# Kernel optimization log

Measured on AMD Instinct MI355X. Metric: run time of the kernel, lower is better.

Reference implementation:

```python
import jax, jax.numpy as jnp
import numpy as np

N_NODES = 100000
N_EDGES = 1600000
ATOM_DIM = 16
POS_DIM = 3
HID = 128


def _linear_init(key, fan_in, fan_out):
    # torch nn.Linear default: U(-1/sqrt(fan_in), 1/sqrt(fan_in)) for W and b
    kw, kb = jax.random.split(key)
    bound = 1.0 / np.sqrt(fan_in)
    W = jax.random.uniform(kw, (fan_in, fan_out), jnp.float32, -bound, bound)
    b = jax.random.uniform(kb, (fan_out,), jnp.float32, -bound, bound)
    return W, b


def setup_inputs() -> dict:
    key = jax.random.key(0)
    ks = jax.random.split(key, 8)
    x = jax.random.normal(ks[0], (N_NODES, ATOM_DIM), jnp.float32)
    pos = jax.random.normal(ks[1], (N_NODES, POS_DIM), jnp.float32)
    edge_index = jax.random.randint(ks[2], (2, N_EDGES), 0, N_NODES, jnp.int64 if jax.config.jax_enable_x64 else jnp.int32)
    Wa, ba = _linear_init(ks[3], ATOM_DIM, HID)
    Wp, bp = _linear_init(ks[4], POS_DIM, HID)
    W1, b1 = _linear_init(ks[5], 2 * HID + 1, HID)
    W2, b2 = _linear_init(ks[6], HID, HID)
    W3, b3 = _linear_init(ks[7], HID, 4)
    return {"x": x, "pos": pos, "edge_index": edge_index,
            "Wa": Wa, "ba": ba, "Wp": Wp, "bp": bp,
            "W1": W1, "b1": b1, "W2": W2, "b2": b2, "W3": W3, "b3": b3}


def reference(x, pos, edge_index, Wa, ba, Wp, bp, W1, b1, W2, b2, W3, b3):
    # node embeddings: atom_emb + pos_emb, [N, HID]
    node_emb = (x @ Wa + ba) + (pos @ Wp + bp)
    src, dst = edge_index[0], edge_index[1]
    source_emb = node_emb[src]            # [E, HID]
    target_emb = node_emb[dst]            # [E, HID]
    diff = pos[src] - pos[dst]            # [E, 3]
    distances = jnp.linalg.norm(diff, axis=-1, keepdims=True)  # [E, 1]
    edge_input = jnp.concatenate([source_emb, target_emb, distances], axis=-1)  # [E, 2*HID+1]
    h = jax.nn.silu(edge_input @ W1 + b1)
    h = jax.nn.silu(h @ W2 + b2)
    bond_logits = h @ W3 + b3             # [E, 4]
    return bond_logits
```

## Files before the change

kernel.cpp:

```cpp
#include <hip/hip_runtime.h>
#include <hip/hip_bf16.h>
#include <hip/hip_fp16.h>

typedef _Float16 half8 __attribute__((ext_vector_type(8)));
typedef _Float16 half4 __attribute__((ext_vector_type(4)));
typedef __fp16 fp16x2 __attribute__((ext_vector_type(2)));
typedef float floatx4 __attribute__((ext_vector_type(4)));

#define HID 128
#define TILE_M 64

__device__ __forceinline__ float fast_silu(float v) {
    float e = __expf(-v);
    return v * __builtin_amdgcn_rcpf(1.f + e);
}

__device__ __forceinline__ unsigned int pk2(float a, float b) {
    fp16x2 h = __builtin_amdgcn_cvt_pkrtz(a, b);
    return __builtin_bit_cast(unsigned int, h);
}

__device__ __forceinline__ void barrier_lds_only() {
    asm volatile("s_waitcnt lgkmcnt(0)\n\ts_barrier" ::: "memory");
}

#define LDO 136
__global__ __launch_bounds__(256) void node_emb_kernel(
    const float* __restrict__ x, const float* __restrict__ pos,
    const float* __restrict__ Wa, const float* __restrict__ ba,
    const float* __restrict__ Wp, const float* __restrict__ bp,
    _Float16* __restrict__ nodeEmb, int N)
{
    __shared__ __align__(16) _Float16 sOut[64 * LDO];
    const int t    = threadIdx.x;
    const int wave = t >> 6;
    const int lane = t & 63;
    const int quad = lane >> 4;
    const int l16  = lane & 15;

    half8 wf[2];
    floatx4 bias[2];
    #pragma unroll
    for (int ct = 0; ct < 2; ++ct) {
        int col = wave * 32 + ct * 16 + l16;
        #pragma unroll
        for (int j = 0; j < 8; ++j) {
            int k = quad * 8 + j;
            float w = 0.f;
            if (k < 16) w = Wa[k * HID + col];
            else if (k < 19) w = Wp[(k - 16) * HID + col];
            wf[ct][j] = (_Float16)w;
        }
        #pragma unroll
        for (int i = 0; i < 4; ++i) {
            int c2 = wave * 32 + ct * 16 + quad * 4 + i;
            bias[ct][i] = ba[c2] + bp[c2];
        }
    }

    int nTiles = (N + 63) >> 6;
    for (int tile = blockIdx.x; tile < nTiles; tile += gridDim.x) {
        int base = tile * 64;
        half8 af[4];
        #pragma unroll
        for (int rt = 0; rt < 4; ++rt) {
            int node = base + rt * 16 + l16;
            int nd = node < N ? node : N - 1;
            half8 a = (half8){0, 0, 0, 0, 0, 0, 0, 0};
            if (quad < 2) {
                const float* xp = x + (size_t)nd * 16 + quad * 8;
                float4 v0 = *(const float4*)xp;
                float4 v1 = *(const float4*)(xp + 4);
                a[0] = (_Float16)v0.x; a[1] = (_Float16)v0.y;
                a[2] = (_Float16)v0.z; a[3] = (_Float16)v0.w;
                a[4] = (_Float16)v1.x; a[5] = (_Float16)v1.y;
                a[6] = (_Float16)v1.z; a[7] = (_Float16)v1.w;
            } else if (quad == 2) {
                const float* pp = pos + (size_t)nd * 3;
                a[0] = (_Float16)pp[0]; a[1] = (_Float16)pp[1]; a[2] = (_Float16)pp[2];
            }
            af[rt] = a;
        }
        #pragma unroll
        for (int ct = 0; ct < 2; ++ct)
            #pragma unroll
            for (int rt = 0; rt < 4; ++rt) {
                floatx4 d = bias[ct];
                d = __builtin_amdgcn_mfma_f32_16x16x32_f16(wf[ct], af[rt], d, 0, 0, 0);
                half4 hv;
                hv[0] = (_Float16)d[0]; hv[1] = (_Float16)d[1];
                hv[2] = (_Float16)d[2]; hv[3] = (_Float16)d[3];
                *(half4*)&sOut[(rt * 16 + l16) * LDO + wave * 32 + ct * 16 + quad * 4] = hv;
            }
        __syncthreads();
        #pragma unroll
        for (int p = 0; p < 4; ++p) {
            int idx = p * 256 + t;
            int r = idx >> 4, c = idx & 15;
            int node = base + r;
            if (node < N)
                *(half8*)(nodeEmb + (size_t)node * HID + c * 8) =
                    *(const half8*)&sOut[r * LDO + c * 8];
        }
        __syncthreads();
    }
}

__global__ __launch_bounds__(256, 2) void edge_mlp_kernel(
    const _Float16* __restrict__ nodeEmb,
    const float* __restrict__ pos,
    const int* __restrict__ eidx,
    const float* __restrict__ W1, const float* __restrict__ b1,
    const float* __restrict__ W2, const float* __restrict__ b2,
    const float* __restrict__ W3, const float* __restrict__ b3,
    float* __restrict__ out, int E, int nTiles)
{
    __shared__ __align__(16) _Float16 sA[2 * TILE_M * HID];
    __shared__ __align__(16) _Float16 sH1[TILE_M * HID];
    __shared__ __align__(16) _Float16 sH2[TILE_M * HID];
    __shared__ float sDist[TILE_M];

    const int t    = threadIdx.x;
    const int wave = t >> 6;
    const int lane = t & 63;
    const int quad = lane >> 4;
    const int l16  = lane & 15;
    const int colbase = wave * 32;

    half8 w1f[8][2];
    half8 w2f[4][2];
    half8 w3f[4];
    float w1c[2][4], b1f[2][4], b2f[2][4];
    #pragma unroll
    for (int ct = 0; ct < 2; ++ct) {
        int col = colbase + ct * 16 + l16;
        #pragma unroll
        for (int kc = 0; kc < 8; ++kc)
            #pragma unroll
            for (int j = 0; j < 8; ++j)
                w1f[kc][ct][j] = (_Float16)W1[(kc * 32 + quad * 8 + j) * HID + col];
        #pragma unroll
        for (int kc = 0; kc < 4; ++kc)
            #pragma unroll
            for (int j = 0; j < 8; ++j)
                w2f[kc][ct][j] = (_Float16)W2[(kc * 32 + quad * 8 + j) * HID + col];
        #pragma unroll
        for (int i = 0; i < 4; ++i) {
            int c2 = colbase + ct * 16 + quad * 4 + i;
            w1c[ct][i] = W1[256 * HID + c2];
            b1f[ct][i] = b1[c2];
            b2f[ct][i] = b2[c2];
        }
    }
    #pragma unroll
    for (int kc = 0; kc < 4; ++kc)
        #pragma unroll
        for (int j = 0; j < 8; ++j)
            w3f[kc][j] = (_Float16)W3[(kc * 32 + quad * 8 + j) * 4 + (l16 & 3)];
    const float b3v0 = b3[0], b3v1 = b3[1], b3v2 = b3[2], b3v3 = b3[3];

    int nid[8];
    float dpre = 0.f;

    auto load_nid = [&](int tl) {
        int eb = tl * TILE_M;
        #pragma unroll
        for (int i = 0; i < 8; ++i) {
            int cid = i * 256 + t;
            int row = cid >> 4;
            int r   = row & 63;
            int e   = eb + r; if (e >= E) e = E - 1;
            nid[i] = (row >> 6) ? eidx[(size_t)E + e] : eidx[e];
        }
    };
    auto load_dist = [&](int tl) -> float {
        if (t >= TILE_M) return 0.f;
        int e = tl * TILE_M + t; if (e >= E) e = E - 1;
        int s = eidx[e], d = eidx[(size_t)E + e];
        float dx = pos[3 * (size_t)s]     - pos[3 * (size_t)d];
        float dy = pos[3 * (size_t)s + 1] - pos[3 * (size_t)d + 1];
        float dz = pos[3 * (size_t)s + 2] - pos[3 * (size_t)d + 2];
        return sqrtf(dx * dx + dy * dy + dz * dz);
    };
    auto dma_issue = [&]() {
        #pragma unroll
        for (int i = 0; i < 8; ++i) {
            int cid = i * 256 + t;
            int row = cid >> 4;
            int cg  = (cid & 15) ^ (row & 15);
            const _Float16* gp = nodeEmb + (size_t)nid[i] * HID + cg * 8;
            __builtin_amdgcn_global_load_lds(
                (__attribute__((address_space(1))) void*)gp,
                (__attribute__((address_space(3))) void*)&sA[(i * 256 + (t & 192)) * 8],
                16, 0, 0);
        }
    };

    bool havePrev = false;
    int prevEbase = 0;
    int tile = blockIdx.x;
    if (tile < nTiles) {
        load_nid(tile);
        dpre = load_dist(tile);
        dma_issue();
    }

    for (; tile < nTiles; tile += gridDim.x) {
        const int ebase = tile * TILE_M;
        if (t < TILE_M) sDist[t] = dpre;
        __syncthreads();

        if (havePrev) {
            floatx4 acc3 = (floatx4){0.f, 0.f, 0.f, 0.f};
            #pragma unroll
            for (int kc = 0; kc < 4; ++kc) {
                int slot = ((kc * 4 + quad) ^ l16) * 8;
                half8 h = *(const half8*)&sH2[(wave * 16 + l16) * HID + slot];
                acc3 = __builtin_amdgcn_mfma_f32_16x16x32_f16(w3f[kc], h, acc3, 0, 0, 0);
            }
            if (quad == 0) {
                int e = prevEbase + wave * 16 + l16;
                if (e < E) {
                    float4 o = {acc3[0] + b3v0, acc3[1] + b3v1,
                                acc3[2] + b3v2, acc3[3] + b3v3};
                    *(float4*)&out[(size_t)e * 4] = o;
                }
            }
        }

        int nxt = tile + gridDim.x;
        if (nxt < nTiles) {
            load_nid(nxt);
            dpre = load_dist(nxt);
        }

        floatx4 acc[2][4];
        #pragma unroll
        for (int ct = 0; ct < 2; ++ct)
            #pragma unroll
            for (int rt = 0; rt < 4; ++rt) {
                acc[ct][rt][0] = b1f[ct][0]; acc[ct][rt][1] = b1f[ct][1];
                acc[ct][rt][2] = b1f[ct][2]; acc[ct][rt][3] = b1f[ct][3];
            }
        #pragma unroll
        for (int kc = 0; kc < 8; ++kc) {
            int hf   = kc >> 2;
            int cg   = (kc & 3) * 4 + quad;
            int slot = (cg ^ l16) * 8;
            const _Float16* base = &sA[(hf * TILE_M + l16) * HID + slot];
            half8 a0 = *(const half8*)(base + 0 * 16 * HID);
            half8 a1 = *(const half8*)(base + 1 * 16 * HID);
            half8 a2 = *(const half8*)(base + 2 * 16 * HID);
            half8 a3 = *(const half8*)(base + 3 * 16 * HID);
            acc[0][0] = __builtin_amdgcn_mfma_f32_16x16x32_f16(w1f[kc][0], a0, acc[0][0], 0, 0, 0);
            acc[0][1] = __builtin_amdgcn_mfma_f32_16x16x32_f16(w1f[kc][0], a1, acc[0][1], 0, 0, 0);
            acc[0][2] = __builtin_amdgcn_mfma_f32_16x16x32_f16(w1f[kc][0], a2, acc[0][2], 0, 0, 0);
            acc[0][3] = __builtin_amdgcn_mfma_f32_16x16x32_f16(w1f[kc][0], a3, acc[0][3], 0, 0, 0);
            acc[1][0] = __builtin_amdgcn_mfma_f32_16x16x32_f16(w1f[kc][1], a0, acc[1][0], 0, 0, 0);
            acc[1][1] = __builtin_amdgcn_mfma_f32_16x16x32_f16(w1f[kc][1], a1, acc[1][1], 0, 0, 0);
            acc[1][2] = __builtin_amdgcn_mfma_f32_16x16x32_f16(w1f[kc][1], a2, acc[1][2], 0, 0, 0);
            acc[1][3] = __builtin_amdgcn_mfma_f32_16x16x32_f16(w1f[kc][1], a3, acc[1][3], 0, 0, 0);
        }
        #pragma unroll
        for (int rt = 0; rt < 4; ++rt) {
            int m = rt * 16 + l16;
            float d = sDist[m];
            #pragma unroll
            for (int ct = 0; ct < 2; ++ct) {
                float v0 = fast_silu(fmaf(d, w1c[ct][0], acc[ct][rt][0]));
                float v1 = fast_silu(fmaf(d, w1c[ct][1], acc[ct][rt][1]));
                float v2 = fast_silu(fmaf(d, w1c[ct][2], acc[ct][rt][2]));
                float v3 = fast_silu(fmaf(d, w1c[ct][3], acc[ct][rt][3]));
                uint2 w;
                w.x = pk2(v0, v1);
                w.y = pk2(v2, v3);
                int cgb  = wave * 4 + ct * 2 + (quad >> 1);
                int slot = cgb ^ l16;
                *(uint2*)&sH1[m * HID + slot * 8 + (quad & 1) * 4] = w;
            }
        }
        barrier_lds_only();

        if (nxt < nTiles) dma_issue();

        floatx4 acc2[2][4];
        #pragma unroll
        for (int ct = 0; ct < 2; ++ct)
            #pragma unroll
            for (int rt = 0; rt < 4; ++rt) {
                acc2[ct][rt][0] = b2f[ct][0]; acc2[ct][rt][1] = b2f[ct][1];
                acc2[ct][rt][2] = b2f[ct][2]; acc2[ct][rt][3] = b2f[ct][3];
            }
        #pragma unroll
        for (int kc = 0; kc < 4; ++kc) {
            int slot = ((kc * 4 + quad) ^ l16) * 8;
            half8 a0 = *(const half8*)&sH1[(0 * 16 + l16) * HID + slot];
            half8 a1 = *(const half8*)&sH1[(1 * 16 + l16) * HID + slot];
            half8 a2 = *(const half8*)&sH1[(2 * 16 + l16) * HID + slot];
            half8 a3 = *(const half8*)&sH1[(3 * 16 + l16) * HID + slot];
            acc2[0][0] = __builtin_amdgcn_mfma_f32_16x16x32_f16(w2f[kc][0], a0, acc2[0][0], 0, 0, 0);
            acc2[0][1] = __builtin_amdgcn_mfma_f32_16x16x32_f16(w2f[kc][0], a1, acc2[0][1], 0, 0, 0);
            acc2[0][2] = __builtin_amdgcn_mfma_f32_16x16x32_f16(w2f[kc][0], a2, acc2[0][2], 0, 0, 0);
            acc2[0][3] = __builtin_amdgcn_mfma_f32_16x16x32_f16(w2f[kc][0], a3, acc2[0][3], 0, 0, 0);
            acc2[1][0] = __builtin_amdgcn_mfma_f32_16x16x32_f16(w2f[kc][1], a0, acc2[1][0], 0, 0, 0);
            acc2[1][1] = __builtin_amdgcn_mfma_f32_16x16x32_f16(w2f[kc][1], a1, acc2[1][1], 0, 0, 0);
            acc2[1][2] = __builtin_amdgcn_mfma_f32_16x16x32_f16(w2f[kc][1], a2, acc2[1][2], 0, 0, 0);
            acc2[1][3] = __builtin_amdgcn_mfma_f32_16x16x32_f16(w2f[kc][1], a3, acc2[1][3], 0, 0, 0);
        }
        #pragma unroll
        for (int rt = 0; rt < 4; ++rt) {
            int m = rt * 16 + l16;
            #pragma unroll
            for (int ct = 0; ct < 2; ++ct) {
                float v0 = fast_silu(acc2[ct][rt][0]);
                float v1 = fast_silu(acc2[ct][rt][1]);
                float v2 = fast_silu(acc2[ct][rt][2]);
                float v3 = fast_silu(acc2[ct][rt][3]);
                uint2 w;
                w.x = pk2(v0, v1);
                w.y = pk2(v2, v3);
                int cgb  = wave * 4 + ct * 2 + (quad >> 1);
                int slot = cgb ^ l16;
                *(uint2*)&sH2[m * HID + slot * 8 + (quad & 1) * 4] = w;
            }
        }
        havePrev = true;
        prevEbase = ebase;
    }

    if (havePrev) {
        __syncthreads();
        floatx4 acc3 = (floatx4){0.f, 0.f, 0.f, 0.f};
        #pragma unroll
        for (int kc = 0; kc < 4; ++kc) {
            int slot = ((kc * 4 + quad) ^ l16) * 8;
            half8 h = *(const half8*)&sH2[(wave * 16 + l16) * HID + slot];
            acc3 = __builtin_amdgcn_mfma_f32_16x16x32_f16(w3f[kc], h, acc3, 0, 0, 0);
        }
        if (quad == 0) {
            int e = prevEbase + wave * 16 + l16;
            if (e < E) {
                float4 o = {acc3[0] + b3v0, acc3[1] + b3v1,
                            acc3[2] + b3v2, acc3[3] + b3v3};
                *(float4*)&out[(size_t)e * 4] = o;
            }
        }
    }
}

extern "C" void kernel_launch(void* const* d_in, const int* in_sizes, int n_in,
                              void* d_out, int out_size, void* d_ws, size_t ws_size,
                              hipStream_t stream) {
    const float* x   = (const float*)d_in[0];
    const float* pos = (const float*)d_in[1];
    const int*  eidx = (const int*)d_in[2];
    const float* Wa = (const float*)d_in[3];
    const float* ba = (const float*)d_in[4];
    const float* Wp = (const float*)d_in[5];
    const float* bp = (const float*)d_in[6];
    const float* W1 = (const float*)d_in[7];
    const float* b1 = (const float*)d_in[8];
    const float* W2 = (const float*)d_in[9];
    const float* b2 = (const float*)d_in[10];
    const float* W3 = (const float*)d_in[11];
    const float* b3 = (const float*)d_in[12];
    float* out = (float*)d_out;

    int N = in_sizes[0] / 16;
    int E = in_sizes[2] / 2;

    _Float16* nodeEmb = (_Float16*)d_ws;

    int nodeTiles = (N + 63) / 64;
    node_emb_kernel<<<nodeTiles, 256, 0, stream>>>(x, pos, Wa, ba, Wp, bp, nodeEmb, N);

    int nTiles = (E + TILE_M - 1) / TILE_M;
    edge_mlp_kernel<<<512, 256, 0, stream>>>(nodeEmb, pos, eidx,
                                             W1, b1, W2, b2, W3, b3,
                                             out, E, nTiles);
}
```

Baseline: 342.8 us.

## Double-buffer edge input tile and alias hidden activations into consumed buffer

The separate H1/H2 shared buffers are removed and the LDS is split into two ping-pong tile buffers of the same total size. The layer-1 and layer-2 activations now overwrite the current tile's gathered node embeddings once layer 1 has read them. This lets the gather of the next tile's embeddings start right after the layer-1 MFMAs, so it overlaps with SiLU, layer 2 and the layer-3 epilogue. It adds an extra barrier per tile and relies on careful aliasing: the previous tile's H2 must be fully read before the new gather overwrites that buffer.

```diff
diff --git a/kernel.cpp b/kernel.cpp
--- a/kernel.cpp
+++ b/kernel.cpp
@@ -9,6 +9,8 @@
 
 #define HID 128
 #define TILE_M 64
+#define TSZ (2 * TILE_M * HID)
+#define H2OFF (TILE_M * HID)
 
 __device__ __forceinline__ float fast_silu(float v) {
     float e = __expf(-v);
@@ -115,9 +117,7 @@
     const float* __restrict__ W3, const float* __restrict__ b3,
     float* __restrict__ out, int E, int nTiles)
 {
-    __shared__ __align__(16) _Float16 sA[2 * TILE_M * HID];
-    __shared__ __align__(16) _Float16 sH1[TILE_M * HID];
-    __shared__ __align__(16) _Float16 sH2[TILE_M * HID];
+    __shared__ __align__(16) _Float16 sA[2 * TSZ];
     __shared__ float sDist[TILE_M];
 
     const int t    = threadIdx.x;
@@ -182,7 +182,7 @@
         float dz = pos[3 * (size_t)s + 2] - pos[3 * (size_t)d + 2];
         return sqrtf(dx * dx + dy * dy + dz * dz);
     };
-    auto dma_issue = [&]() {
+    auto dma_issue = [&](_Float16* dst) {
         #pragma unroll
         for (int i = 0; i < 8; ++i) {
             int cid = i * 256 + t;
@@ -191,22 +191,26 @@
             const _Float16* gp = nodeEmb + (size_t)nid[i] * HID + cg * 8;
             __builtin_amdgcn_global_load_lds(
                 (__attribute__((address_space(1))) void*)gp,
-                (__attribute__((address_space(3))) void*)&sA[(i * 256 + (t & 192)) * 8],
+                (__attribute__((address_space(3))) void*)&dst[(i * 256 + (t & 192)) * 8],
                 16, 0, 0);
         }
     };
 
     bool havePrev = false;
     int prevEbase = 0;
+    int cur = 0;
+    int prevBuf = 0;
     int tile = blockIdx.x;
     if (tile < nTiles) {
         load_nid(tile);
         dpre = load_dist(tile);
-        dma_issue();
+        dma_issue(sA);
     }
 
     for (; tile < nTiles; tile += gridDim.x) {
         const int ebase = tile * TILE_M;
+        _Float16* bufC = sA + cur * TSZ;
+        _Float16* bufP = sA + (cur ^ 1) * TSZ;
         if (t < TILE_M) sDist[t] = dpre;
         __syncthreads();
 
@@ -215,7 +219,7 @@
             #pragma unroll
             for (int kc = 0; kc < 4; ++kc) {
                 int slot = ((kc * 4 + quad) ^ l16) * 8;
-                half8 h = *(const half8*)&sH2[(wave * 16 + l16) * HID + slot];
+                half8 h = *(const half8*)&bufP[H2OFF + (wave * 16 + l16) * HID + slot];
                 acc3 = __builtin_amdgcn_mfma_f32_16x16x32_f16(w3f[kc], h, acc3, 0, 0, 0);
             }
             if (quad == 0) {
@@ -247,7 +251,7 @@
             int hf   = kc >> 2;
             int cg   = (kc & 3) * 4 + quad;
             int slot = (cg ^ l16) * 8;
-            const _Float16* base = &sA[(hf * TILE_M + l16) * HID + slot];
+            const _Float16* base = &bufC[(hf * TILE_M + l16) * HID + slot];
             half8 a0 = *(const half8*)(base + 0 * 16 * HID);
             half8 a1 = *(const half8*)(base + 1 * 16 * HID);
             half8 a2 = *(const half8*)(base + 2 * 16 * HID);
@@ -261,6 +265,10 @@
             acc[1][2] = __builtin_amdgcn_mfma_f32_16x16x32_f16(w1f[kc][1], a2, acc[1][2], 0, 0, 0);
             acc[1][3] = __builtin_amdgcn_mfma_f32_16x16x32_f16(w1f[kc][1], a3, acc[1][3], 0, 0, 0);
         }
+        barrier_lds_only();
+
+        if (nxt < nTiles) dma_issue(bufP);
+
         #pragma unroll
         for (int rt = 0; rt < 4; ++rt) {
             int m = rt * 16 + l16;
@@ -276,12 +284,10 @@
                 w.y = pk2(v2, v3);
                 int cgb  = wave * 4 + ct * 2 + (quad >> 1);
                 int slot = cgb ^ l16;
-                *(uint2*)&sH1[m * HID + slot * 8 + (quad & 1) * 4] = w;
+                *(uint2*)&bufC[m * HID + slot * 8 + (quad & 1) * 4] = w;
             }
         }
         barrier_lds_only();
-
-        if (nxt < nTiles) dma_issue();
 
         floatx4 acc2[2][4];
         #pragma unroll
@@ -294,10 +300,10 @@
         #pragma unroll
         for (int kc = 0; kc < 4; ++kc) {
             int slot = ((kc * 4 + quad) ^ l16) * 8;
-            half8 a0 = *(const half8*)&sH1[(0 * 16 + l16) * HID + slot];
-            half8 a1 = *(const half8*)&sH1[(1 * 16 + l16) * HID + slot];
-            half8 a2 = *(const half8*)&sH1[(2 * 16 + l16) * HID + slot];
-            half8 a3 = *(const half8*)&sH1[(3 * 16 + l16) * HID + slot];
+            half8 a0 = *(const half8*)&bufC[(0 * 16 + l16) * HID + slot];
+            half8 a1 = *(const half8*)&bufC[(1 * 16 + l16) * HID + slot];
+            half8 a2 = *(const half8*)&bufC[(2 * 16 + l16) * HID + slot];
+            half8 a3 = *(const half8*)&bufC[(3 * 16 + l16) * HID + slot];
             acc2[0][0] = __builtin_amdgcn_mfma_f32_16x16x32_f16(w2f[kc][0], a0, acc2[0][0], 0, 0, 0);
             acc2[0][1] = __builtin_amdgcn_mfma_f32_16x16x32_f16(w2f[kc][0], a1, acc2[0][1], 0, 0, 0);
             acc2[0][2] = __builtin_amdgcn_mfma_f32_16x16x32_f16(w2f[kc][0], a2, acc2[0][2], 0, 0, 0);
@@ -307,6 +313,7 @@
             acc2[1][2] = __builtin_amdgcn_mfma_f32_16x16x32_f16(w2f[kc][1], a2, acc2[1][2], 0, 0, 0);
             acc2[1][3] = __builtin_amdgcn_mfma_f32_16x16x32_f16(w2f[kc][1], a3, acc2[1][3], 0, 0, 0);
         }
+
         #pragma unroll
         for (int rt = 0; rt < 4; ++rt) {
             int m = rt * 16 + l16;
@@ -321,20 +328,23 @@
                 w.y = pk2(v2, v3);
                 int cgb  = wave * 4 + ct * 2 + (quad >> 1);
                 int slot = cgb ^ l16;
-                *(uint2*)&sH2[m * HID + slot * 8 + (quad & 1) * 4] = w;
+                *(uint2*)&bufC[H2OFF + m * HID + slot * 8 + (quad & 1) * 4] = w;
             }
         }
         havePrev = true;
         prevEbase = ebase;
+        prevBuf = cur;
+        cur ^= 1;
     }
 
     if (havePrev) {
         __syncthreads();
+        const _Float16* bufL = sA + prevBuf * TSZ;
         floatx4 acc3 = (floatx4){0.f, 0.f, 0.f, 0.f};
         #pragma unroll
         for (int kc = 0; kc < 4; ++kc) {
             int slot = ((kc * 4 + quad) ^ l16) * 8;
-            half8 h = *(const half8*)&sH2[(wave * 16 + l16) * HID + slot];
+            half8 h = *(const half8*)&bufL[H2OFF + (wave * 16 + l16) * HID + slot];
             acc3 = __builtin_amdgcn_mfma_f32_16x16x32_f16(w3f[kc], h, acc3, 0, 0, 0);
         }
         if (quad == 0) {
```

New measurement: 355.5 us. 1.04x slower.

## Split edge MLP columns across eight waves and move W3 fragments to LDS

Applied to the files above, without the earlier changes.

The edge MLP block grows from 256 to 512 threads, so each wave owns 16 output columns instead of 32. This halves the per-thread W1/W2 register fragments and accumulators. W3 fragments are staged once in shared memory rather than held in registers, and only the first four waves run the final layer. The goal is lower register pressure and more resident waves per CU to hide gather and MFMA latency. In exchange each A tile is read from LDS by twice as many waves, and the grid stays at 512 blocks.

```diff
diff --git a/kernel.cpp b/kernel.cpp
--- a/kernel.cpp
+++ b/kernel.cpp
@@ -106,7 +106,7 @@
     }
 }
 
-__global__ __launch_bounds__(256, 2) void edge_mlp_kernel(
+__global__ __launch_bounds__(512, 4) void edge_mlp_kernel(
     const _Float16* __restrict__ nodeEmb,
     const float* __restrict__ pos,
     const int* __restrict__ eidx,
@@ -119,54 +119,56 @@
     __shared__ __align__(16) _Float16 sH1[TILE_M * HID];
     __shared__ __align__(16) _Float16 sH2[TILE_M * HID];
     __shared__ float sDist[TILE_M];
+    __shared__ __align__(16) _Float16 sW3[512];
 
     const int t    = threadIdx.x;
     const int wave = t >> 6;
     const int lane = t & 63;
     const int quad = lane >> 4;
     const int l16  = lane & 15;
-    const int colbase = wave * 32;
-
-    half8 w1f[8][2];
-    half8 w2f[4][2];
-    half8 w3f[4];
-    float w1c[2][4], b1f[2][4], b2f[2][4];
-    #pragma unroll
-    for (int ct = 0; ct < 2; ++ct) {
-        int col = colbase + ct * 16 + l16;
+    const int colbase = wave * 16;
+
+    if (t < 64) {
+        int kc = t >> 4, q = (t >> 2) & 3, c = t & 3;
+        #pragma unroll
+        for (int j = 0; j < 8; ++j)
+            sW3[(kc * 16 + q * 4 + c) * 8 + j] =
+                (_Float16)W3[(kc * 32 + q * 8 + j) * 4 + c];
+    }
+
+    half8 w1f[8];
+    half8 w2f[4];
+    float w1c[4], b1f[4], b2f[4];
+    {
+        int col = colbase + l16;
         #pragma unroll
         for (int kc = 0; kc < 8; ++kc)
             #pragma unroll
             for (int j = 0; j < 8; ++j)
-                w1f[kc][ct][j] = (_Float16)W1[(kc * 32 + quad * 8 + j) * HID + col];
+                w1f[kc][j] = (_Float16)W1[(kc * 32 + quad * 8 + j) * HID + col];
         #pragma unroll
         for (int kc = 0; kc < 4; ++kc)
             #pragma unroll
             for (int j = 0; j < 8; ++j)
-                w2f[kc][ct][j] = (_Float16)W2[(kc * 32 + quad * 8 + j) * HID + col];
+                w2f[kc][j] = (_Float16)W2[(kc * 32 + quad * 8 + j) * HID + col];
         #pragma unroll
         for (int i = 0; i < 4; ++i) {
-            int c2 = colbase + ct * 16 + quad * 4 + i;
-            w1c[ct][i] = W1[256 * HID + c2];
-            b1f[ct][i] = b1[c2];
-            b2f[ct][i] = b2[c2];
-        }
-    }
-    #pragma unroll
-    for (int kc = 0; kc < 4; ++kc)
-        #pragma unroll
-        for (int j = 0; j < 8; ++j)
-            w3f[kc][j] = (_Float16)W3[(kc * 32 + quad * 8 + j) * 4 + (l16 & 3)];
+            int c2 = colbase + quad * 4 + i;
+            w1c[i] = W1[256 * HID + c2];
+            b1f[i] = b1[c2];
+            b2f[i] = b2[c2];
+        }
+    }
     const float b3v0 = b3[0], b3v1 = b3[1], b3v2 = b3[2], b3v3 = b3[3];
 
-    int nid[8];
+    int nid[4];
     float dpre = 0.f;
 
     auto load_nid = [&](int tl) {
         int eb = tl * TILE_M;
         #pragma unroll
-        for (int i = 0; i < 8; ++i) {
-            int cid = i * 256 + t;
+        for (int i = 0; i < 4; ++i) {
+            int cid = i * 512 + t;
             int row = cid >> 4;
             int r   = row & 63;
             int e   = eb + r; if (e >= E) e = E - 1;
@@ -184,14 +186,14 @@
     };
     auto dma_issue = [&]() {
         #pragma unroll
-        for (int i = 0; i < 8; ++i) {
-            int cid = i * 256 + t;
+        for (int i = 0; i < 4; ++i) {
+            int cid = i * 512 + t;
             int row = cid >> 4;
             int cg  = (cid & 15) ^ (row & 15);
             const _Float16* gp = nodeEmb + (size_t)nid[i] * HID + cg * 8;
             __builtin_amdgcn_global_load_lds(
                 (__attribute__((address_space(1))) void*)gp,
-                (__attribute__((address_space(3))) void*)&sA[(i * 256 + (t & 192)) * 8],
+                (__attribute__((address_space(3))) void*)&sA[(i * 512 + (t & 448)) * 8],
                 16, 0, 0);
         }
     };
@@ -210,13 +212,14 @@
         if (t < TILE_M) sDist[t] = dpre;
         __syncthreads();
 
-        if (havePrev) {
+        if (havePrev && wave < 4) {
             floatx4 acc3 = (floatx4){0.f, 0.f, 0.f, 0.f};
             #pragma unroll
             for (int kc = 0; kc < 4; ++kc) {
                 int slot = ((kc * 4 + quad) ^ l16) * 8;
-                half8 h = *(const half8*)&sH2[(wave * 16 + l16) * HID + slot];
-                acc3 = __builtin_amdgcn_mfma_f32_16x16x32_f16(w3f[kc], h, acc3, 0, 0, 0);
+                half8 h  = *(const half8*)&sH2[(wave * 16 + l16) * HID + slot];
+                half8 w3 = *(const half8*)&sW3[(kc * 16 + quad * 4 + (l16 & 3)) * 8];
+                acc3 = __builtin_amdgcn_mfma_f32_16x16x32_f16(w3, h, acc3, 0, 0, 0);
             }
             if (quad == 0) {
                 int e = prevEbase + wave * 16 + l16;
@@ -234,14 +237,12 @@
             dpre = load_dist(nxt);
         }
 
-        floatx4 acc[2][4];
-        #pragma unroll
-        for (int ct = 0; ct < 2; ++ct)
-            #pragma unroll
-            for (int rt = 0; rt < 4; ++rt) {
-                acc[ct][rt][0] = b1f[ct][0]; acc[ct][rt][1] = b1f[ct][1];
-                acc[ct][rt][2] = b1f[ct][2]; acc[ct][rt][3] = b1f[ct][3];
-            }
+        floatx4 acc[4];
+        #pragma unroll
+        for (int rt = 0; rt < 4; ++rt) {
+            acc[rt][0] = b1f[0]; acc[rt][1] = b1f[1];
+            acc[rt][2] = b1f[2]; acc[rt][3] = b1f[3];
+        }
         #pragma unroll
         for (int kc = 0; kc < 8; ++kc) {
             int hf   = kc >> 2;
@@ -252,45 +253,36 @@
             half8 a1 = *(const half8*)(base + 1 * 16 * HID);
             half8 a2 = *(const half8*)(base + 2 * 16 * HID);
             half8 a3 = *(const half8*)(base + 3 * 16 * HID);
-            acc[0][0] = __builtin_amdgcn_mfma_f32_16x16x32_f16(w1f[kc][0], a0, acc[0][0], 0, 0, 0);
-            acc[0][1] = __builtin_amdgcn_mfma_f32_16x16x32_f16(w1f[kc][0], a1, acc[0][1], 0, 0, 0);
-            acc[0][2] = __builtin_amdgcn_mfma_f32_16x16x32_f16(w1f[kc][0], a2, acc[0][2], 0, 0, 0);
-            acc[0][3] = __builtin_amdgcn_mfma_f32_16x16x32_f16(w1f[kc][0], a3, acc[0][3], 0, 0, 0);
-            acc[1][0] = __builtin_amdgcn_mfma_f32_16x16x32_f16(w1f[kc][1], a0, acc[1][0], 0, 0, 0);
-            acc[1][1] = __builtin_amdgcn_mfma_f32_16x16x32_f16(w1f[kc][1], a1, acc[1][1], 0, 0, 0);
-            acc[1][2] = __builtin_amdgcn_mfma_f32_16x16x32_f16(w1f[kc][1], a2, acc[1][2], 0, 0, 0);
-            acc[1][3] = __builtin_amdgcn_mfma_f32_16x16x32_f16(w1f[kc][1], a3, acc[1][3], 0, 0, 0);
+            acc[0] = __builtin_amdgcn_mfma_f32_16x16x32_f16(w1f[kc], a0, acc[0], 0, 0, 0);
+            acc[1] = __builtin_amdgcn_mfma_f32_16x16x32_f16(w1f[kc], a1, acc[1], 0, 0, 0);
+            acc[2] = __builtin_amdgcn_mfma_f32_16x16x32_f16(w1f[kc], a2, acc[2], 0, 0, 0);
+            acc[3] = __builtin_amdgcn_mfma_f32_16x16x32_f16(w1f[kc], a3, acc[3], 0, 0, 0);
         }
         #pragma unroll
         for (int rt = 0; rt < 4; ++rt) {
             int m = rt * 16 + l16;
             float d = sDist[m];
-            #pragma unroll
-            for (int ct = 0; ct < 2; ++ct) {
-                float v0 = fast_silu(fmaf(d, w1c[ct][0], acc[ct][rt][0]));
-                float v1 = fast_silu(fmaf(d, w1c[ct][1], acc[ct][rt][1]));
-                float v2 = fast_silu(fmaf(d, w1c[ct][2], acc[ct][rt][2]));
-                float v3 = fast_silu(fmaf(d, w1c[ct][3], acc[ct][rt][3]));
-                uint2 w;
-                w.x = pk2(v0, v1);
-                w.y = pk2(v2, v3);
-                int cgb  = wave * 4 + ct * 2 + (quad >> 1);
-                int slot = cgb ^ l16;
-                *(uint2*)&sH1[m * HID + slot * 8 + (quad & 1) * 4] = w;
-            }
+            float v0 = fast_silu(fmaf(d, w1c[0], acc[rt][0]));
+            float v1 = fast_silu(fmaf(d, w1c[1], acc[rt][1]));
+            float v2 = fast_silu(fmaf(d, w1c[2], acc[rt][2]));
+            float v3 = fast_silu(fmaf(d, w1c[3], acc[rt][3]));
+            uint2 w;
+            w.x = pk2(v0, v1);
+            w.y = pk2(v2, v3);
+            int cgb  = wave * 2 + (quad >> 1);
+            int slot = cgb ^ l16;
+            *(uint2*)&sH1[m * HID + slot * 8 + (quad & 1) * 4] = w;
         }
         barrier_lds_only();
 
         if (nxt < nTiles) dma_issue();
 
-        floatx4 acc2[2][4];
-        #pragma unroll
-        for (int ct = 0; ct < 2; ++ct)
-            #pragma unroll
-            for (int rt = 0; rt < 4; ++rt) {
-                acc2[ct][rt][0] = b2f[ct][0]; acc2[ct][rt][1] = b2f[ct][1];
-                acc2[ct][rt][2] = b2f[ct][2]; acc2[ct][rt][3] = b2f[ct][3];
-            }
+        floatx4 acc2[4];
+        #pragma unroll
+        for (int rt = 0; rt < 4; ++rt) {
+            acc2[rt][0] = b2f[0]; acc2[rt][1] = b2f[1];
+            acc2[rt][2] = b2f[2]; acc2[rt][3] = b2f[3];
+        }
         #pragma unroll
         for (int kc = 0; kc < 4; ++kc) {
             int slot = ((kc * 4 + quad) ^ l16) * 8;
@@ -298,31 +290,24 @@
             half8 a1 = *(const half8*)&sH1[(1 * 16 + l16) * HID + slot];
             half8 a2 = *(const half8*)&sH1[(2 * 16 + l16) * HID + slot];
             half8 a3 = *(const half8*)&sH1[(3 * 16 + l16) * HID + slot];
-            acc2[0][0] = __builtin_amdgcn_mfma_f32_16x16x32_f16(w2f[kc][0], a0, acc2[0][0], 0, 0, 0);
-            acc2[0][1] = __builtin_amdgcn_mfma_f32_16x16x32_f16(w2f[kc][0], a1, acc2[0][1], 0, 0, 0);
-            acc2[0][2] = __builtin_amdgcn_mfma_f32_16x16x32_f16(w2f[kc][0], a2, acc2[0][2], 0, 0, 0);
-            acc2[0][3] = __builtin_amdgcn_mfma_f32_16x16x32_f16(w2f[kc][0], a3, acc2[0][3], 0, 0, 0);
-            acc2[1][0] = __builtin_amdgcn_mfma_f32_16x16x32_f16(w2f[kc][1], a0, acc2[1][0], 0, 0, 0);
-            acc2[1][1] = __builtin_amdgcn_mfma_f32_16x16x32_f16(w2f[kc][1], a1, acc2[1][1], 0, 0, 0);
-            acc2[1][2] = __builtin_amdgcn_mfma_f32_16x16x32_f16(w2f[kc][1], a2, acc2[1][2], 0, 0, 0);
-            acc2[1][3] = __builtin_amdgcn_mfma_f32_16x16x32_f16(w2f[kc][1], a3, acc2[1][3], 0, 0, 0);
+            acc2[0] = __builtin_amdgcn_mfma_f32_16x16x32_f16(w2f[kc], a0, acc2[0], 0, 0, 0);
+            acc2[1] = __builtin_amdgcn_mfma_f32_16x16x32_f16(w2f[kc], a1, acc2[1], 0, 0, 0);
+            acc2[2] = __builtin_amdgcn_mfma_f32_16x16x32_f16(w2f[kc], a2, acc2[2], 0, 0, 0);
+            acc2[3] = __builtin_amdgcn_mfma_f32_16x16x32_f16(w2f[kc], a3, acc2[3], 0, 0, 0);
         }
         #pragma unroll
         for (int rt = 0; rt < 4; ++rt) {
             int m = rt * 16 + l16;
-            #pragma unroll
-            for (int ct = 0; ct < 2; ++ct) {
-                float v0 = fast_silu(acc2[ct][rt][0]);
-                float v1 = fast_silu(acc2[ct][rt][1]);
-                float v2 = fast_silu(acc2[ct][rt][2]);
-                float v3 = fast_silu(acc2[ct][rt][3]);
-                uint2 w;
-                w.x = pk2(v0, v1);
-                w.y = pk2(v2, v3);
-                int cgb  = wave * 4 + ct * 2 + (quad >> 1);
-                int slot = cgb ^ l16;
-                *(uint2*)&sH2[m * HID + slot * 8 + (quad & 1) * 4] = w;
-            }
+            float v0 = fast_silu(acc2[rt][0]);
+            float v1 = fast_silu(acc2[rt][1]);
+            float v2 = fast_silu(acc2[rt][2]);
+            float v3 = fast_silu(acc2[rt][3]);
+            uint2 w;
+            w.x = pk2(v0, v1);
+            w.y = pk2(v2, v3);
+            int cgb  = wave * 2 + (quad >> 1);
+            int slot = cgb ^ l16;
+            *(uint2*)&sH2[m * HID + slot * 8 + (quad & 1) * 4] = w;
         }
         havePrev = true;
         prevEbase = ebase;
@@ -330,19 +315,22 @@
 
     if (havePrev) {
         __syncthreads();
-        floatx4 acc3 = (floatx4){0.f, 0.f, 0.f, 0.f};
-        #pragma unroll
-        for (int kc = 0; kc < 4; ++kc) {
-            int slot = ((kc * 4 + quad) ^ l16) * 8;
-            half8 h = *(const half8*)&sH2[(wave * 16 + l16) * HID + slot];
-            acc3 = __builtin_amdgcn_mfma_f32_16x16x32_f16(w3f[kc], h, acc3, 0, 0, 0);
-        }
-        if (quad == 0) {
-            int e = prevEbase + wave * 16 + l16;
-            if (e < E) {
-                float4 o = {acc3[0] + b3v0, acc3[1] + b3v1,
-                            acc3[2] + b3v2, acc3[3] + b3v3};
-                *(float4*)&out[(size_t)e * 4] = o;
+        if (wave < 4) {
+            floatx4 acc3 = (floatx4){0.f, 0.f, 0.f, 0.f};
+            #pragma unroll
+            for (int kc = 0; kc < 4; ++kc) {
+                int slot = ((kc * 4 + quad) ^ l16) * 8;
+                half8 h  = *(const half8*)&sH2[(wave * 16 + l16) * HID + slot];
+                half8 w3 = *(const half8*)&sW3[(kc * 16 + quad * 4 + (l16 & 3)) * 8];
+                acc3 = __builtin_amdgcn_mfma_f32_16x16x32_f16(w3, h, acc3, 0, 0, 0);
+            }
+            if (quad == 0) {
+                int e = prevEbase + wave * 16 + l16;
+                if (e < E) {
+                    float4 o = {acc3[0] + b3v0, acc3[1] + b3v1,
+                                acc3[2] + b3v2, acc3[3] + b3v3};
+                    *(float4*)&out[(size_t)e * 4] = o;
+                }
             }
         }
     }
@@ -375,7 +363,7 @@
     node_emb_kernel<<<nodeTiles, 256, 0, stream>>>(x, pos, Wa, ba, Wp, bp, nodeEmb, N);
 
     int nTiles = (E + TILE_M - 1) / TILE_M;
-    edge_mlp_kernel<<<512, 256, 0, stream>>>(nodeEmb, pos, eidx,
+    edge_mlp_kernel<<<512, 512, 0, stream>>>(nodeEmb, pos, eidx,
                                              W1, b1, W2, b2, W3, b3,
                                              out, E, nTiles);
 }
```

After: 331.1 us (median of 2 runs). 1.04x faster.
